# Optimization experiments

Measured on AMD Instinct MI355X. Metric: run time of the kernel, lower is better.

## Reference

```python
import jax, jax.numpy as jnp
import numpy as np

B, S, D_IN = 2, 2048, 1024
EMBED, HEADS = 1024, 16
HEAD_DIM = EMBED // HEADS

def setup_inputs() -> dict:
    key = jax.random.key(0)
    k1, k2, k3 = jax.random.split(key, 3)
    # xavier_uniform bounds
    def xavier(k, shape):
        fan_in, fan_out = shape[1], shape[0]
        lim = jnp.sqrt(6.0 / (fan_in + fan_out))
        return jax.random.uniform(k, shape, jnp.float32, -lim, lim)
    x = jax.random.normal(k1, (B, S, D_IN), jnp.float32)
    qkv_w = xavier(k2, (3 * EMBED, D_IN))   # torch Linear weight layout [out, in]
    qkv_b = jnp.zeros((3 * EMBED,), jnp.float32)
    o_w = xavier(k3, (EMBED, EMBED))
    o_b = jnp.zeros((EMBED,), jnp.float32)
    return {"x": x, "qkv_w": qkv_w, "qkv_b": qkv_b, "o_w": o_w, "o_b": o_b}

def reference(x, qkv_w, qkv_b, o_w, o_b):
    Bq, Sq, _ = x.shape
    qkv = x @ qkv_w.T + qkv_b                       # [B,S,3E]
    qkv = qkv.reshape(Bq, Sq, HEADS, 3 * HEAD_DIM).transpose(0, 2, 1, 3)  # [B,H,S,3d]
    q, k, v = jnp.split(qkv, 3, axis=-1)            # each [B,H,S,d]
    scale = 1.0 / jnp.sqrt(jnp.asarray(HEAD_DIM, x.dtype))
    logits = jnp.einsum('bhqd,bhkd->bhqk', q, k) * scale
    attn = jax.nn.softmax(logits, axis=-1)
    vals = jnp.einsum('bhqk,bhkd->bhqd', attn, v)   # [B,H,S,d]
    vals = vals.transpose(0, 2, 1, 3).reshape(Bq, Sq, EMBED)
    return vals @ o_w.T + o_b
```

## Files before the change

kernel.cpp:

```cpp
#include <hip/hip_runtime.h>
#include <hip/hip_bf16.h>

#define B_    2
#define S_    2048
#define DIN   1024
#define EMB   1024
#define NH    16
#define HD    64
#define N3    3072
#define MROWS 4096
#define KVB   64
#define QBLK  128
#define NT    (S_ / KVB)

typedef short bf16x8 __attribute__((ext_vector_type(8)));
typedef float f32x4  __attribute__((ext_vector_type(4)));
typedef float f32x16 __attribute__((ext_vector_type(16)));
typedef unsigned short u16;
typedef u16 u16x8 __attribute__((ext_vector_type(8)));
typedef u16 u16x4 __attribute__((ext_vector_type(4)));
typedef unsigned int u32;

__device__ __forceinline__ u16 f2bf(float f) {
  union { float f; unsigned u; } x; x.f = f;
  unsigned r = x.u + 0x7fffu + ((x.u >> 16) & 1u);
  return (u16)(r >> 16);
}

__device__ __forceinline__ u32 cvtpk(float lo, float hi) {
  u32 r;
  asm("v_cvt_pk_bf16_f32 %0, %1, %2" : "=v"(r) : "v"(lo), "v"(hi));
  return r;
}

__device__ __forceinline__ void gload16(const void* g, void* l) {
  __builtin_amdgcn_global_load_lds(
      (const __attribute__((address_space(1))) unsigned int*)g,
      (__attribute__((address_space(3))) unsigned int*)l, 16, 0, 0);
}

#define BARRIER() do { asm volatile("" ::: "memory"); \
                       __builtin_amdgcn_s_barrier();  \
                       asm volatile("" ::: "memory"); } while (0)

__global__ __launch_bounds__(256)
void cast_all(const float* __restrict__ x, const float* __restrict__ w1,
              const float* __restrict__ w2, u16* __restrict__ ox,
              u16* __restrict__ ow1, u16* __restrict__ ow2) {
  const int i = blockIdx.x * 256 + threadIdx.x;
  const float* src; u16* dst; int off;
  if (i < 1048576)              { src = x;  dst = ox;  off = i; }
  else if (i < 1048576 + 786432){ src = w1; dst = ow1; off = i - 1048576; }
  else                          { src = w2; dst = ow2; off = i - 1835008; }
  const float4 v = ((const float4*)src)[off];
  u16x4 o;
  o[0] = f2bf(v.x); o[1] = f2bf(v.y); o[2] = f2bf(v.z); o[3] = f2bf(v.w);
  ((u16x4*)dst)[off] = o;
}

template<int EPI>
__global__ __launch_bounds__(256)
void gemm_bt(const u16* __restrict__ A, const u16* __restrict__ W,
             const float* __restrict__ bias, float* __restrict__ Cf,
             u16* __restrict__ Qb, u16* __restrict__ Kb, u16* __restrict__ VbT,
             int M, int N, int K) {
  __shared__ u16 Als[2][128 * 32];
  __shared__ u16 Bls[2][128 * 32];
  const int tid  = threadIdx.x;
  const int wave = tid >> 6, lane = tid & 63;
  const int lhi  = lane >> 4, llo = lane & 15;
  const int wr   = wave >> 1, wc = wave & 1;
  const int m0   = blockIdx.y * 128, n0 = blockIdx.x * 128;
  const int KT   = K >> 5;

  f32x4 acc[4][4];
#pragma unroll
  for (int m = 0; m < 4; ++m)
#pragma unroll
    for (int n = 0; n < 4; ++n) acc[m][n] = f32x4{0.f, 0.f, 0.f, 0.f};

  auto issue = [&](int t) {
#pragma unroll
    for (int i = 0; i < 2; ++i) {
      const int e   = (tid + i * 256) * 8;
      const int row = e >> 5, col = e & 31;
      gload16(A + (size_t)(m0 + row) * K + t * 32 + col,
              (char*)Als[t & 1] + wave * 1024 + i * 4096);
      gload16(W + (size_t)(n0 + row) * K + t * 32 + col,
              (char*)Bls[t & 1] + wave * 1024 + i * 4096);
    }
  };

  issue(0);
  for (int t = 0; t < KT; ++t) {
    if (t + 1 < KT) {
      issue(t + 1);
      asm volatile("s_waitcnt vmcnt(4)" ::: "memory");
    } else {
      asm volatile("s_waitcnt vmcnt(0)" ::: "memory");
    }
    BARRIER();
    const u16* Ab = Als[t & 1];
    const u16* Bb = Bls[t & 1];
    bf16x8 af[4], bfr[4];
#pragma unroll
    for (int m = 0; m < 4; ++m) af[m]  = *(const bf16x8*)&Ab[(wr * 64 + m * 16 + llo) * 32 + lhi * 8];
#pragma unroll
    for (int n = 0; n < 4; ++n) bfr[n] = *(const bf16x8*)&Bb[(wc * 64 + n * 16 + llo) * 32 + lhi * 8];
#pragma unroll
    for (int m = 0; m < 4; ++m)
#pragma unroll
      for (int n = 0; n < 4; ++n)
        acc[m][n] = __builtin_amdgcn_mfma_f32_16x16x32_bf16(af[m], bfr[n], acc[m][n], 0, 0, 0);
    BARRIER();
  }

#pragma unroll
  for (int n = 0; n < 4; ++n) {
    const int colb = n0 + wc * 64 + n * 16;
    const int gcol = colb + llo;
    const float bv = bias[gcol];
    if (EPI == 0) {
      const int h   = colb / 192;
      const int rr  = colb - h * 192;
      const int sec = rr >> 6;
      const int d   = (rr & 63) + llo;
#pragma unroll
      for (int m = 0; m < 4; ++m) {
        const int rowb = m0 + wr * 64 + m * 16 + lhi * 4;
        const int b = rowb >> 11, s0 = rowb & 2047;
        if (sec == 2) {
          u16x4 vv;
#pragma unroll
          for (int r = 0; r < 4; ++r) vv[r] = f2bf(acc[m][n][r] + bv);
          *(u16x4*)&VbT[((size_t)(b * NH + h) * HD + d) * S_ + s0] = vv;
        } else {
          u16* dst = (sec == 0) ? Qb : Kb;
          const float scl = (sec == 0) ? 0.18033688f : 1.0f;
#pragma unroll
          for (int r = 0; r < 4; ++r)
            dst[(((size_t)(b * NH + h) * S_ + s0 + r) << 6) + d] = f2bf((acc[m][n][r] + bv) * scl);
        }
      }
    } else {
#pragma unroll
      for (int m = 0; m < 4; ++m) {
        const int rowb = m0 + wr * 64 + m * 16 + lhi * 4;
#pragma unroll
        for (int r = 0; r < 4; ++r)
          Cf[(size_t)(rowb + r) * N + gcol] = acc[m][n][r] + bv;
      }
    }
  }
}

__global__ __launch_bounds__(256, 2)
void attn_fwd(const u16* __restrict__ Qb, const u16* __restrict__ Kb,
              const u16* __restrict__ VbT, u16* __restrict__ Obf) {
  __shared__ __align__(16) u16 Kls[4][KVB * HD];
  __shared__ __align__(16) u16 Vls[4][HD * KVB];
  __shared__ __align__(16) float sBc[4][32];
  const int tid  = threadIdx.x;
  const int wave = tid >> 6, lane = tid & 63;
  const int q    = lane & 31, hi = lane >> 5;
  const int bh   = blockIdx.y;
  const int q0   = blockIdx.x * QBLK;
  const size_t base  = (size_t)bh * S_ * HD;
  const size_t basev = (size_t)bh * HD * S_;

  const int qrow = q0 + wave * 32 + q;
  bf16x8 qf[4];
#pragma unroll
  for (int c = 0; c < 4; ++c)
    qf[c] = *(const bf16x8*)&Qb[base + (size_t)qrow * HD + c * 16 + hi * 8];

  const int srow = tid >> 3;
  const int xs   = (tid & 7) ^ (srow & 7);
  const u16* kSrc = Kb  + base  + (size_t)srow * HD + xs * 8;
  const u16* vSrc = VbT + basev + (size_t)srow * S_ + xs * 8;
  const int ldsW = wave * 1024;

  const int gq = 16 * (q >> 4) + 8 * ((q >> 2) & 1) + (q & 3) + 4 * ((q >> 3) & 1);
  int offK[2][4], offV[2][4];
#pragma unroll
  for (int b = 0; b < 2; ++b)
#pragma unroll
    for (int c = 0; c < 4; ++c) {
      offK[b][c] = (b * 32 + gq) * 128 + (((c * 2 + hi) ^ (gq & 7)) << 4);
      offV[b][c] = (b * 32 + q)  * 128 + (((c * 2 + hi) ^ (q  & 7)) << 4);
    }

  f32x16 o0, o1, z16;
#pragma unroll
  for (int r = 0; r < 16; ++r) { o0[r] = 0.f; o1[r] = 0.f; z16[r] = 0.f; }
  float m_run = -1e30f, lsum = 0.f;

  auto issue = [&](int t) {
#pragma unroll
    for (int p = 0; p < 2; ++p) {
      gload16(kSrc + (size_t)t * KVB * HD + (size_t)p * 32 * HD,
              (char*)Kls[t & 3] + p * 4096 + ldsW);
      gload16(vSrc + t * KVB + (size_t)p * 32 * S_,
              (char*)Vls[t & 3] + p * 4096 + ldsW);
    }
  };

  auto qk = [&](int t, f32x16& s0, f32x16& s1) {
    const char* Kt = (const char*)Kls[t & 3];
    {
      bf16x8 k0 = *(const bf16x8*)(Kt + offK[0][0]);
      bf16x8 k1 = *(const bf16x8*)(Kt + offK[1][0]);
      s0 = __builtin_amdgcn_mfma_f32_32x32x16_bf16(k0, qf[0], z16, 0, 0, 0);
      s1 = __builtin_amdgcn_mfma_f32_32x32x16_bf16(k1, qf[0], z16, 0, 0, 0);
    }
#pragma unroll
    for (int c = 1; c < 4; ++c) {
      bf16x8 k0 = *(const bf16x8*)(Kt + offK[0][c]);
      bf16x8 k1 = *(const bf16x8*)(Kt + offK[1][c]);
      s0 = __builtin_amdgcn_mfma_f32_32x32x16_bf16(k0, qf[c], s0, 0, 0, 0);
      s1 = __builtin_amdgcn_mfma_f32_32x32x16_bf16(k1, qf[c], s1, 0, 0, 0);
    }
  };

  auto sm = [&](f32x16& s0, f32x16& s1, u32 (&dw0)[8], u32 (&dw1)[8]) {
    float tm[16];
#pragma unroll
    for (int r = 0; r < 16; ++r) tm[r] = fmaxf(s0[r], s1[r]);
#pragma unroll
    for (int st = 8; st >= 1; st >>= 1)
#pragma unroll
      for (int i = 0; i < 16; ++i) if (i < st) tm[i] = fmaxf(tm[i], tm[i + st]);
    const float pm = fmaxf(tm[0], __shfl_xor(tm[0], 32));

    if (__any(pm > m_run + 10.0f)) {
      const float mnew  = fmaxf(m_run, pm);
      const float alpha = exp2f(m_run - mnew);
      sBc[wave][q] = alpha;
      asm volatile("s_waitcnt lgkmcnt(0)" ::: "memory");
      f32x4 av[4];
#pragma unroll
      for (int g = 0; g < 4; ++g) av[g] = *(const f32x4*)&sBc[wave][hi * 4 + g * 8];
#pragma unroll
      for (int r = 0; r < 16; ++r) {
        const float f = av[r >> 2][r & 3];
        o0[r] *= f; o1[r] *= f;
      }
      lsum *= alpha;
      m_run = mnew;
    }

    float t0 = 0.f, t1 = 0.f, t2 = 0.f, t3 = 0.f;
#pragma unroll
    for (int j = 0; j < 8; ++j) {
      const float a0 = exp2f(s0[2 * j] - m_run), a1 = exp2f(s0[2 * j + 1] - m_run);
      const float b0 = exp2f(s1[2 * j] - m_run), b1 = exp2f(s1[2 * j + 1] - m_run);
      t0 += a0; t1 += a1; t2 += b0; t3 += b1;
      dw0[j] = cvtpk(a0, a1);
      dw1[j] = cvtpk(b0, b1);
    }
    float ts = (t0 + t1) + (t2 + t3);
    ts += __shfl_xor(ts, 32);
    lsum += ts;
  };

  auto pv = [&](int t, u32 (&dw0)[8], u32 (&dw1)[8]) {
    const char* Vt = (const char*)Vls[t & 3];
#pragma unroll
    for (int c = 0; c < 4; ++c) {
      union { u32 u[4]; bf16x8 v; } P;
      if (c == 0)      { P.u[0] = dw0[0]; P.u[1] = dw0[1]; P.u[2] = dw0[2]; P.u[3] = dw0[3]; }
      else if (c == 1) { P.u[0] = dw0[4]; P.u[1] = dw0[5]; P.u[2] = dw0[6]; P.u[3] = dw0[7]; }
      else if (c == 2) { P.u[0] = dw1[0]; P.u[1] = dw1[1]; P.u[2] = dw1[2]; P.u[3] = dw1[3]; }
      else             { P.u[0] = dw1[4]; P.u[1] = dw1[5]; P.u[2] = dw1[6]; P.u[3] = dw1[7]; }
      bf16x8 v0 = *(const bf16x8*)(Vt + offV[0][c]);
      bf16x8 v1 = *(const bf16x8*)(Vt + offV[1][c]);
      o0 = __builtin_amdgcn_mfma_f32_32x32x16_bf16(P.v, v0, o0, 0, 0, 0);
      o1 = __builtin_amdgcn_mfma_f32_32x32x16_bf16(P.v, v1, o1, 0, 0, 0);
    }
  };

  f32x16 sE0, sE1, sO0, sO1;
  u32 dwE0[8], dwE1[8], dwO0[8], dwO1[8];

  issue(0); issue(1);
  for (int p = 0; p < NT / 2 - 1; ++p) {
    issue(2 * p + 2); issue(2 * p + 3);
    asm volatile("s_waitcnt vmcnt(8)" ::: "memory");
    BARRIER();
    qk(2 * p,     sE0, sE1);
    qk(2 * p + 1, sO0, sO1);
    sm(sE0, sE1, dwE0, dwE1);
    pv(2 * p,     dwE0, dwE1);
    sm(sO0, sO1, dwO0, dwO1);
    pv(2 * p + 1, dwO0, dwO1);
    BARRIER();
  }
  asm volatile("s_waitcnt vmcnt(0)" ::: "memory");
  BARRIER();
  qk(NT - 2, sE0, sE1);
  qk(NT - 1, sO0, sO1);
  sm(sE0, sE1, dwE0, dwE1);
  pv(NT - 2, dwE0, dwE1);
  sm(sO0, sO1, dwO0, dwO1);
  pv(NT - 1, dwO0, dwO1);

  const float li = 1.0f / lsum;
  sBc[wave][q] = li;
  asm volatile("s_waitcnt lgkmcnt(0)" ::: "memory");
  f32x4 lv[4];
#pragma unroll
  for (int g = 0; g < 4; ++g) lv[g] = *(const f32x4*)&sBc[wave][hi * 4 + g * 8];
  const int b = bh >> 4, h = bh & 15;
#pragma unroll
  for (int r = 0; r < 16; ++r) {
    const int qg = q0 + wave * 32 + (r & 3) + 8 * (r >> 2) + 4 * hi;
    const float f = lv[r >> 2][r & 3];
    u16* dst = Obf + ((size_t)(b * S_ + qg) * NH + h) * HD;
    dst[q]      = f2bf(o0[r] * f);
    dst[32 + q] = f2bf(o1[r] * f);
  }
}

extern "C" void kernel_launch(void* const* d_in, const int* in_sizes, int n_in,
                              void* d_out, int out_size, void* d_ws, size_t ws_size,
                              hipStream_t stream) {
  const float* x     = (const float*)d_in[0];
  const float* qkv_w = (const float*)d_in[1];
  const float* qkv_b = (const float*)d_in[2];
  const float* o_w   = (const float*)d_in[3];
  const float* o_b   = (const float*)d_in[4];
  float* out = (float*)d_out;

  char* ws = (char*)d_ws;
  u16* xbf  = (u16*)(ws);
  u16* wqkv = (u16*)(ws + (8u  << 20));
  u16* wo   = (u16*)(ws + (14u << 20));
  u16* Qb   = (u16*)(ws + (16u << 20));
  u16* Kb   = (u16*)(ws + (24u << 20));
  u16* VbT  = (u16*)(ws + (32u << 20));
  u16* atnb = xbf;

  cast_all<<<8192, 256, 0, stream>>>(x, qkv_w, o_w, xbf, wqkv, wo);

  gemm_bt<0><<<dim3(N3 / 128, MROWS / 128), 256, 0, stream>>>(
      xbf, wqkv, qkv_b, nullptr, Qb, Kb, VbT, MROWS, N3, DIN);

  attn_fwd<<<dim3(S_ / QBLK, B_ * NH), 256, 0, stream>>>(Qb, Kb, VbT, atnb);

  gemm_bt<1><<<dim3(EMB / 128, MROWS / 128), 256, 0, stream>>>(
      atnb, wo, o_b, out, nullptr, nullptr, nullptr, MROWS, EMB, EMB);
}
```

Measured before the change: 132.6 us.

## Triple-buffer GEMM global loads and remap attention blocks for XCD locality

The GEMM K-loop moves from double to triple buffering in LDS, issuing loads two tiles ahead with adjusted vmcnt waits so memory latency is better hidden behind MFMA work. The attention launch becomes a 1D grid whose block index is remapped so that blocks of the same batch-head land on the same XCD (bid&7), which is meant to improve L2 reuse of K/V. The extra LDS buffer raises shared memory per block and may reduce occupancy.

```diff
diff --git a/kernel.cpp b/kernel.cpp
--- a/kernel.cpp
+++ b/kernel.cpp
@@ -64,8 +64,8 @@
              const float* __restrict__ bias, float* __restrict__ Cf,
              u16* __restrict__ Qb, u16* __restrict__ Kb, u16* __restrict__ VbT,
              int M, int N, int K) {
-  __shared__ u16 Als[2][128 * 32];
-  __shared__ u16 Bls[2][128 * 32];
+  __shared__ u16 Als[3][128 * 32];
+  __shared__ u16 Bls[3][128 * 32];
   const int tid  = threadIdx.x;
   const int wave = tid >> 6, lane = tid & 63;
   const int lhi  = lane >> 4, llo = lane & 15;
@@ -80,28 +80,21 @@
     for (int n = 0; n < 4; ++n) acc[m][n] = f32x4{0.f, 0.f, 0.f, 0.f};
 
   auto issue = [&](int t) {
+    const int buf = t % 3;
 #pragma unroll
     for (int i = 0; i < 2; ++i) {
       const int e   = (tid + i * 256) * 8;
       const int row = e >> 5, col = e & 31;
       gload16(A + (size_t)(m0 + row) * K + t * 32 + col,
-              (char*)Als[t & 1] + wave * 1024 + i * 4096);
+              (char*)Als[buf] + wave * 1024 + i * 4096);
       gload16(W + (size_t)(n0 + row) * K + t * 32 + col,
-              (char*)Bls[t & 1] + wave * 1024 + i * 4096);
-    }
-  };
-
-  issue(0);
-  for (int t = 0; t < KT; ++t) {
-    if (t + 1 < KT) {
-      issue(t + 1);
-      asm volatile("s_waitcnt vmcnt(4)" ::: "memory");
-    } else {
-      asm volatile("s_waitcnt vmcnt(0)" ::: "memory");
-    }
-    BARRIER();
-    const u16* Ab = Als[t & 1];
-    const u16* Bb = Bls[t & 1];
+              (char*)Bls[buf] + wave * 1024 + i * 4096);
+    }
+  };
+
+  auto compute = [&](int t) {
+    const u16* Ab = Als[t % 3];
+    const u16* Bb = Bls[t % 3];
     bf16x8 af[4], bfr[4];
 #pragma unroll
     for (int m = 0; m < 4; ++m) af[m]  = *(const bf16x8*)&Ab[(wr * 64 + m * 16 + llo) * 32 + lhi * 8];
@@ -112,8 +105,20 @@
 #pragma unroll
       for (int n = 0; n < 4; ++n)
         acc[m][n] = __builtin_amdgcn_mfma_f32_16x16x32_bf16(af[m], bfr[n], acc[m][n], 0, 0, 0);
+  };
+
+  issue(0); issue(1);
+  for (int t = 0; t < KT - 2; ++t) {
+    issue(t + 2);
+    asm volatile("s_waitcnt vmcnt(8)" ::: "memory");
+    BARRIER();
+    compute(t);
     BARRIER();
   }
+  asm volatile("s_waitcnt vmcnt(4)" ::: "memory");
+  BARRIER(); compute(KT - 2); BARRIER();
+  asm volatile("s_waitcnt vmcnt(0)" ::: "memory");
+  BARRIER(); compute(KT - 1);
 
 #pragma unroll
   for (int n = 0; n < 4; ++n) {
@@ -163,8 +168,10 @@
   const int tid  = threadIdx.x;
   const int wave = tid >> 6, lane = tid & 63;
   const int q    = lane & 31, hi = lane >> 5;
-  const int bh   = blockIdx.y;
-  const int q0   = blockIdx.x * QBLK;
+  const int bid  = blockIdx.x;
+  const int g    = bid >> 3;
+  const int bh   = (bid & 7) * 4 + (g >> 4);
+  const int q0   = (g & 15) * QBLK;
   const size_t base  = (size_t)bh * S_ * HD;
   const size_t basev = (size_t)bh * HD * S_;
 
@@ -239,7 +246,7 @@
       asm volatile("s_waitcnt lgkmcnt(0)" ::: "memory");
       f32x4 av[4];
 #pragma unroll
-      for (int g = 0; g < 4; ++g) av[g] = *(const f32x4*)&sBc[wave][hi * 4 + g * 8];
+      for (int gg = 0; gg < 4; ++gg) av[gg] = *(const f32x4*)&sBc[wave][hi * 4 + gg * 8];
 #pragma unroll
       for (int r = 0; r < 16; ++r) {
         const float f = av[r >> 2][r & 3];
@@ -309,7 +316,7 @@
   asm volatile("s_waitcnt lgkmcnt(0)" ::: "memory");
   f32x4 lv[4];
 #pragma unroll
-  for (int g = 0; g < 4; ++g) lv[g] = *(const f32x4*)&sBc[wave][hi * 4 + g * 8];
+  for (int gg = 0; gg < 4; ++gg) lv[gg] = *(const f32x4*)&sBc[wave][hi * 4 + gg * 8];
   const int b = bh >> 4, h = bh & 15;
 #pragma unroll
   for (int r = 0; r < 16; ++r) {
@@ -345,7 +352,7 @@
   gemm_bt<0><<<dim3(N3 / 128, MROWS / 128), 256, 0, stream>>>(
       xbf, wqkv, qkv_b, nullptr, Qb, Kb, VbT, MROWS, N3, DIN);
 
-  attn_fwd<<<dim3(S_ / QBLK, B_ * NH), 256, 0, stream>>>(Qb, Kb, VbT, atnb);
+  attn_fwd<<<512, 256, 0, stream>>>(Qb, Kb, VbT, atnb);
 
   gemm_bt<1><<<dim3(EMB / 128, MROWS / 128), 256, 0, stream>>>(
       atnb, wo, o_b, out, nullptr, nullptr, nullptr, MROWS, EMB, EMB);
```

Result: slower. 138.0 us (+4.1%).

## Use 64-row tiles for output GEMM and remap attention blocks for XCD locality

Applied to the files above, without the earlier changes.

The output projection GEMM becomes a separate kernel with 64x128 tiles, which doubles its block count from 256 to 512 and gives better CU occupancy on the 256-CU part. The attention grid is flattened to 1D, and block IDs are remapped so the 8 round-robin XCDs each get consecutive (batch, head) groups, improving L2 reuse of K/V. The QKV GEMM is specialised to a non-template kernel with constant K. Smaller tiles lower per-block arithmetic intensity and raise global traffic for the weight matrix.

```diff
diff --git a/kernel.cpp b/kernel.cpp
--- a/kernel.cpp
+++ b/kernel.cpp
@@ -58,14 +58,13 @@
   ((u16x4*)dst)[off] = o;
 }
 
-template<int EPI>
 __global__ __launch_bounds__(256)
-void gemm_bt(const u16* __restrict__ A, const u16* __restrict__ W,
-             const float* __restrict__ bias, float* __restrict__ Cf,
-             u16* __restrict__ Qb, u16* __restrict__ Kb, u16* __restrict__ VbT,
-             int M, int N, int K) {
+void gemm_qkv(const u16* __restrict__ A, const u16* __restrict__ W,
+              const float* __restrict__ bias,
+              u16* __restrict__ Qb, u16* __restrict__ Kb, u16* __restrict__ VbT) {
   __shared__ u16 Als[2][128 * 32];
   __shared__ u16 Bls[2][128 * 32];
+  const int K = DIN;
   const int tid  = threadIdx.x;
   const int wave = tid >> 6, lane = tid & 63;
   const int lhi  = lane >> 4, llo = lane & 15;
@@ -120,36 +119,98 @@
     const int colb = n0 + wc * 64 + n * 16;
     const int gcol = colb + llo;
     const float bv = bias[gcol];
-    if (EPI == 0) {
-      const int h   = colb / 192;
-      const int rr  = colb - h * 192;
-      const int sec = rr >> 6;
-      const int d   = (rr & 63) + llo;
-#pragma unroll
-      for (int m = 0; m < 4; ++m) {
-        const int rowb = m0 + wr * 64 + m * 16 + lhi * 4;
-        const int b = rowb >> 11, s0 = rowb & 2047;
-        if (sec == 2) {
-          u16x4 vv;
-#pragma unroll
-          for (int r = 0; r < 4; ++r) vv[r] = f2bf(acc[m][n][r] + bv);
-          *(u16x4*)&VbT[((size_t)(b * NH + h) * HD + d) * S_ + s0] = vv;
-        } else {
-          u16* dst = (sec == 0) ? Qb : Kb;
-          const float scl = (sec == 0) ? 0.18033688f : 1.0f;
-#pragma unroll
-          for (int r = 0; r < 4; ++r)
-            dst[(((size_t)(b * NH + h) * S_ + s0 + r) << 6) + d] = f2bf((acc[m][n][r] + bv) * scl);
-        }
+    const int h   = colb / 192;
+    const int rr  = colb - h * 192;
+    const int sec = rr >> 6;
+    const int d   = (rr & 63) + llo;
+#pragma unroll
+    for (int m = 0; m < 4; ++m) {
+      const int rowb = m0 + wr * 64 + m * 16 + lhi * 4;
+      const int b = rowb >> 11, s0 = rowb & 2047;
+      if (sec == 2) {
+        u16x4 vv;
+#pragma unroll
+        for (int r = 0; r < 4; ++r) vv[r] = f2bf(acc[m][n][r] + bv);
+        *(u16x4*)&VbT[((size_t)(b * NH + h) * HD + d) * S_ + s0] = vv;
+      } else {
+        u16* dst = (sec == 0) ? Qb : Kb;
+        const float scl = (sec == 0) ? 0.18033688f : 1.0f;
+#pragma unroll
+        for (int r = 0; r < 4; ++r)
+          dst[(((size_t)(b * NH + h) * S_ + s0 + r) << 6) + d] = f2bf((acc[m][n][r] + bv) * scl);
       }
+    }
+  }
+}
+
+__global__ __launch_bounds__(256)
+void gemm_out_m64(const u16* __restrict__ A, const u16* __restrict__ W,
+                  const float* __restrict__ bias, float* __restrict__ Cf,
+                  int M, int N, int K) {
+  __shared__ u16 Als[2][64 * 32];
+  __shared__ u16 Bls[2][128 * 32];
+  const int tid  = threadIdx.x;
+  const int wave = tid >> 6, lane = tid & 63;
+  const int lhi  = lane >> 4, llo = lane & 15;
+  const int wr   = wave >> 1, wc = wave & 1;
+  const int m0   = blockIdx.y * 64, n0 = blockIdx.x * 128;
+  const int KT   = K >> 5;
+
+  f32x4 acc[2][4];
+#pragma unroll
+  for (int m = 0; m < 2; ++m)
+#pragma unroll
+    for (int n = 0; n < 4; ++n) acc[m][n] = f32x4{0.f, 0.f, 0.f, 0.f};
+
+  auto issue = [&](int t) {
+    {
+      const int row = tid >> 2, col = (tid & 3) * 8;
+      gload16(A + (size_t)(m0 + row) * K + t * 32 + col,
+              (char*)Als[t & 1] + wave * 1024);
+    }
+#pragma unroll
+    for (int i = 0; i < 2; ++i) {
+      const int e   = (tid + i * 256) * 8;
+      const int row = e >> 5, col = e & 31;
+      gload16(W + (size_t)(n0 + row) * K + t * 32 + col,
+              (char*)Bls[t & 1] + wave * 1024 + i * 4096);
+    }
+  };
+
+  issue(0);
+  for (int t = 0; t < KT; ++t) {
+    if (t + 1 < KT) {
+      issue(t + 1);
+      asm volatile("s_waitcnt vmcnt(3)" ::: "memory");
     } else {
-#pragma unroll
-      for (int m = 0; m < 4; ++m) {
-        const int rowb = m0 + wr * 64 + m * 16 + lhi * 4;
-#pragma unroll
-        for (int r = 0; r < 4; ++r)
-          Cf[(size_t)(rowb + r) * N + gcol] = acc[m][n][r] + bv;
-      }
+      asm volatile("s_waitcnt vmcnt(0)" ::: "memory");
+    }
+    BARRIER();
+    const u16* Ab = Als[t & 1];
+    const u16* Bb = Bls[t & 1];
+    bf16x8 af[2], bfr[4];
+#pragma unroll
+    for (int m = 0; m < 2; ++m) af[m]  = *(const bf16x8*)&Ab[(wr * 32 + m * 16 + llo) * 32 + lhi * 8];
+#pragma unroll
+    for (int n = 0; n < 4; ++n) bfr[n] = *(const bf16x8*)&Bb[(wc * 64 + n * 16 + llo) * 32 + lhi * 8];
+#pragma unroll
+    for (int m = 0; m < 2; ++m)
+#pragma unroll
+      for (int n = 0; n < 4; ++n)
+        acc[m][n] = __builtin_amdgcn_mfma_f32_16x16x32_bf16(af[m], bfr[n], acc[m][n], 0, 0, 0);
+    BARRIER();
+  }
+
+#pragma unroll
+  for (int n = 0; n < 4; ++n) {
+    const int gcol = n0 + wc * 64 + n * 16 + llo;
+    const float bv = bias[gcol];
+#pragma unroll
+    for (int m = 0; m < 2; ++m) {
+      const int rowb = m0 + wr * 32 + m * 16 + lhi * 4;
+#pragma unroll
+      for (int r = 0; r < 4; ++r)
+        Cf[(size_t)(rowb + r) * N + gcol] = acc[m][n][r] + bv;
     }
   }
 }
@@ -163,8 +224,10 @@
   const int tid  = threadIdx.x;
   const int wave = tid >> 6, lane = tid & 63;
   const int q    = lane & 31, hi = lane >> 5;
-  const int bh   = blockIdx.y;
-  const int q0   = blockIdx.x * QBLK;
+  const int bid  = blockIdx.x;
+  const int g    = bid >> 3;
+  const int bh   = (bid & 7) * 4 + (g >> 4);
+  const int q0   = (g & 15) * QBLK;
   const size_t base  = (size_t)bh * S_ * HD;
   const size_t basev = (size_t)bh * HD * S_;
 
@@ -239,7 +302,7 @@
       asm volatile("s_waitcnt lgkmcnt(0)" ::: "memory");
       f32x4 av[4];
 #pragma unroll
-      for (int g = 0; g < 4; ++g) av[g] = *(const f32x4*)&sBc[wave][hi * 4 + g * 8];
+      for (int gg = 0; gg < 4; ++gg) av[gg] = *(const f32x4*)&sBc[wave][hi * 4 + gg * 8];
 #pragma unroll
       for (int r = 0; r < 16; ++r) {
         const float f = av[r >> 2][r & 3];
@@ -309,7 +372,7 @@
   asm volatile("s_waitcnt lgkmcnt(0)" ::: "memory");
   f32x4 lv[4];
 #pragma unroll
-  for (int g = 0; g < 4; ++g) lv[g] = *(const f32x4*)&sBc[wave][hi * 4 + g * 8];
+  for (int gg = 0; gg < 4; ++gg) lv[gg] = *(const f32x4*)&sBc[wave][hi * 4 + gg * 8];
   const int b = bh >> 4, h = bh & 15;
 #pragma unroll
   for (int r = 0; r < 16; ++r) {
@@ -342,11 +405,11 @@
 
   cast_all<<<8192, 256, 0, stream>>>(x, qkv_w, o_w, xbf, wqkv, wo);
 
-  gemm_bt<0><<<dim3(N3 / 128, MROWS / 128), 256, 0, stream>>>(
-      xbf, wqkv, qkv_b, nullptr, Qb, Kb, VbT, MROWS, N3, DIN);
-
-  attn_fwd<<<dim3(S_ / QBLK, B_ * NH), 256, 0, stream>>>(Qb, Kb, VbT, atnb);
-
-  gemm_bt<1><<<dim3(EMB / 128, MROWS / 128), 256, 0, stream>>>(
-      atnb, wo, o_b, out, nullptr, nullptr, nullptr, MROWS, EMB, EMB);
-}
+  gemm_qkv<<<dim3(N3 / 128, MROWS / 128), 256, 0, stream>>>(
+      xbf, wqkv, qkv_b, Qb, Kb, VbT);
+
+  attn_fwd<<<512, 256, 0, stream>>>(Qb, Kb, VbT, atnb);
+
+  gemm_out_m64<<<dim3(EMB / 128, MROWS / 64), 256, 0, stream>>>(
+      atnb, wo, o_b, out, MROWS, EMB, EMB);
+}
```

After: 132.1 us. Within noise of the previous version (-0.4%).
